# Kernel optimization log

Hardware: AMD Instinct MI355X
Metric: run time of the kernel (lower is better)

## Reference

```python
import jax, jax.numpy as jnp
import numpy as np

B, S, D, E, K = 4, 4096, 2048, 64, 2
LN_EPS = 1e-5
TEMP_EPS = 1e-6
Z_LOSS_COEF = 0.001
LB_COEF = 0.1


def setup_inputs() -> dict:
    key = jax.random.key(0)
    k1, k2 = jax.random.split(key)
    x = jax.random.normal(k1, (B, S, D), dtype=jnp.float32)
    # kaiming_normal fan_in (std = 1/sqrt(D)) scaled by 0.01, as in __init__
    W = jax.random.normal(k2, (E, D), dtype=jnp.float32) * jnp.float32(0.01 / np.sqrt(D))
    gamma = jnp.ones((E,), jnp.float32)   # LayerNorm weight
    beta = jnp.zeros((E,), jnp.float32)   # LayerNorm bias
    temperature = jnp.full((1,), 0.5, jnp.float32)
    return {"x": x, "W": W, "gamma": gamma, "beta": beta, "temperature": temperature}


def reference(x, W, gamma, beta, temperature):
    b, s, d = x.shape
    xf = x.reshape(-1, d)                                  # [N, D]
    logits = xf @ W.T                                      # [N, E]
    # LayerNorm over expert dim (biased variance, eps=1e-5, matches torch)
    mu = logits.mean(axis=-1, keepdims=True)
    var = jnp.mean(jnp.square(logits - mu), axis=-1, keepdims=True)
    logits = (logits - mu) * jax.lax.rsqrt(var + LN_EPS) * gamma + beta
    # temperature-scaled softmax
    routing_weights = jax.nn.softmax(logits / (temperature + TEMP_EPS), axis=-1)  # [N, E]
    # top-k + scatter into dense dispatch mask
    top_w, top_idx = jax.lax.top_k(routing_weights, K)     # [N, K]
    n = routing_weights.shape[0]
    dispatch = jnp.zeros_like(routing_weights).at[jnp.arange(n)[:, None], top_idx].set(top_w)
    dispatch = dispatch.reshape(b, s, E)                   # [B, S, E]
    # aux losses
    expert_load = dispatch.mean(axis=1)                    # [B, E]
    load_balance_loss = jnp.std(expert_load, ddof=1) / expert_load.mean() * 10.0
    router_z_loss = jnp.mean(jnp.square(logits))
    total_loss = ZLC * router_z_loss + LB_COEF * load_balance_loss if False else (
        Z_LOSS_COEF * router_z_loss + LB_COEF * load_balance_loss)
    return jax.lax.stop_gradient(routing_weights), dispatch, total_loss
```

## Files before the change

### kernel.cpp

```cpp
#include <hip/hip_runtime.h>
#include <hip/hip_bf16.h>
#include <float.h>
#include <math.h>

#define B_DIM 4
#define S_DIM 4096
#define D_DIM 2048
#define E_DIM 64
#define N_TOK 16384
#define TOKS 32
#define NBLK (N_TOK / TOKS)
#define NTHR 512
#define SLICES 4
#define DSLICE (D_DIM / SLICES)
#define KSTEPS2 16
#define GAP_THRESH 1e-3f
#define MAXFLAG 16

typedef __bf16 bf16x8_t __attribute__((ext_vector_type(8)));
typedef float f32x4_t __attribute__((ext_vector_type(4)));

union U8 { bf16x8_t v; unsigned short u[8]; };

__device__ __forceinline__ void split2(float f, unsigned short& h, unsigned short& l) {
    unsigned int u = __float_as_uint(f);
    h = (unsigned short)(u >> 16);
    float hf = __uint_as_float(u & 0xFFFF0000u);
    l = (unsigned short)(__float_as_uint(f - hf) >> 16);
}

typedef const __attribute__((address_space(1))) unsigned int* gas1_t;
typedef __attribute__((address_space(3))) unsigned int* las3_t;
__device__ __forceinline__ void gll16(const unsigned short* g, unsigned short* l) {
    __builtin_amdgcn_global_load_lds((gas1_t)(const void*)g, (las3_t)(void*)l, 16, 0, 0);
}

__global__ void wsplit(const float* __restrict__ W, unsigned short* __restrict__ wh,
                       unsigned short* __restrict__ wl, float* __restrict__ wshdr) {
    const int i = blockIdx.x * 256 + threadIdx.x;
    if (blockIdx.x == 0) { wshdr[threadIdx.x] = 0.f; wshdr[threadIdx.x + 256] = 0.f; }
    const int e    = i >> 8;
    const int k8   = i & 255;
    const int quad = k8 & 3;
    const int h    = (k8 >> 2) & 1;
    const int s    = (k8 >> 3) & 7;
    const int sl   = k8 >> 6;
    const int t    = e >> 4;
    const int l15  = e & 15;
    const int lane = quad * 16 + l15;
    const size_t f = ((size_t)((sl * 8 + s) * 2 + h) * 4 + t) * 64 + lane;
    float4 a = *(const float4*)(W + (size_t)e * D_DIM + k8 * 8);
    float4 b = *(const float4*)(W + (size_t)e * D_DIM + k8 * 8 + 4);
    ushort4 h0, l0, h1, l1;
    split2(a.x, h0.x, l0.x); split2(a.y, h0.y, l0.y);
    split2(a.z, h0.z, l0.z); split2(a.w, h0.w, l0.w);
    split2(b.x, h1.x, l1.x); split2(b.y, h1.y, l1.y);
    split2(b.z, h1.z, l1.z); split2(b.w, h1.w, l1.w);
    *(ushort4*)(wh + f * 8)     = h0;
    *(ushort4*)(wh + f * 8 + 4) = h1;
    *(ushort4*)(wl + f * 8)     = l0;
    *(ushort4*)(wl + f * 8 + 4) = l1;
}

__global__ __launch_bounds__(NTHR, 4) void router_main(
    const float* __restrict__ x, const float* __restrict__ W,
    const unsigned short* __restrict__ whg, const unsigned short* __restrict__ wlg,
    const float* __restrict__ gamma, const float* __restrict__ beta,
    const float* __restrict__ temperature,
    float* __restrict__ out_rw, float* __restrict__ out_dp,
    float* __restrict__ g_zsum, float* __restrict__ g_load)
{
    __shared__ __align__(16) unsigned char arena[65536];
    unsigned short* const bufH = (unsigned short*)arena;
    unsigned short* const bufL = (unsigned short*)(arena + 32768);
    float (* const part)[TOKS][E_DIM + 2] = (float (*)[TOKS][E_DIM + 2])arena;
    float (* const lgt)[E_DIM + 1] = (float (*)[E_DIM + 1])(arena + 33792);

    __shared__ float lgm[E_DIM], lbt[E_DIM], loadsum[E_DIM];
    __shared__ float smu[TOKS], srs[TOKS], sinv[TOKS];
    __shared__ int sel1[TOKS], sel2[TOKS];
    __shared__ int ftok[MAXFLAG], fcand[MAXFLAG][3];
    __shared__ int nflag;

    const int tid = threadIdx.x;
    const int tokBase = blockIdx.x * TOKS;
    const int lane = tid & 63;
    const int wv = tid >> 6;
    const int g  = wv & 1;
    const int sl = wv >> 1;
    const int l15 = lane & 15;
    const int quad = lane >> 4;

    if (tid == 0) nflag = 0;
    if (tid < E_DIM) { lgm[tid] = gamma[tid]; lbt[tid] = beta[tid]; loadsum[tid] = 0.f; }

    const float* xp = x + (size_t)(tokBase + g * 16 + l15) * D_DIM + sl * DSLICE + quad * 8;

    const int kk0  = tid >> 8;
    const int soff = (tid & 255) * 8;

    f32x4_t acc[4];
    #pragma unroll
    for (int t = 0; t < 4; ++t) acc[t] = (f32x4_t){0.f, 0.f, 0.f, 0.f};

#define STAGE(S2, B) do {                                                          \
        const size_t gof = (size_t)(S2) * 2048 + soff;                             \
        unsigned short* hB = bufH + (B) * 8192;                                    \
        unsigned short* lB = bufL + (B) * 8192;                                    \
        gll16(whg + (size_t)kk0 * 32768 + gof,       hB + kk0 * 2048 + soff);      \
        gll16(wlg + (size_t)kk0 * 32768 + gof,       lB + kk0 * 2048 + soff);      \
        gll16(whg + (size_t)(kk0 + 2) * 32768 + gof, hB + (kk0 + 2) * 2048 + soff);\
        gll16(wlg + (size_t)(kk0 + 2) * 32768 + gof, lB + (kk0 + 2) * 2048 + soff);\
    } while (0)

    STAGE(0, 0);
    float4 xq0 = *(const float4*)(xp);
    float4 xq1 = *(const float4*)(xp + 4);
    __syncthreads();

    for (int s2 = 0; s2 < KSTEPS2; ++s2) {
        const int cur = s2 & 1;
        const bool more = (s2 + 1 < KSTEPS2);
        float4 xn0, xn1;
        if (more) {
            STAGE(s2 + 1, cur ^ 1);
            xn0 = *(const float4*)(xp + (s2 + 1) * 32);
            xn1 = *(const float4*)(xp + (s2 + 1) * 32 + 4);
        }
        const unsigned short* hb = bufH + cur * 8192 + sl * 2048;
        const unsigned short* lb = bufL + cur * 8192 + sl * 2048;
        bf16x8_t bh[4], bl[4];
        #pragma unroll
        for (int t = 0; t < 4; ++t) {
            bh[t] = *(const bf16x8_t*)(hb + t * 512 + lane * 8);
            bl[t] = *(const bf16x8_t*)(lb + t * 512 + lane * 8);
        }
        float tf[8] = {xq0.x, xq0.y, xq0.z, xq0.w, xq1.x, xq1.y, xq1.z, xq1.w};
        U8 ah, al;
        #pragma unroll
        for (int k = 0; k < 8; ++k) split2(tf[k], ah.u[k], al.u[k]);
        #pragma unroll
        for (int t = 0; t < 4; ++t) {
            acc[t] = __builtin_amdgcn_mfma_f32_16x16x32_bf16(ah.v, bh[t], acc[t], 0, 0, 0);
            acc[t] = __builtin_amdgcn_mfma_f32_16x16x32_bf16(ah.v, bl[t], acc[t], 0, 0, 0);
            acc[t] = __builtin_amdgcn_mfma_f32_16x16x32_bf16(al.v, bh[t], acc[t], 0, 0, 0);
        }
        if (more) { xq0 = xn0; xq1 = xn1; }
        __syncthreads();
    }
#undef STAGE

    #pragma unroll
    for (int t = 0; t < 4; ++t)
        #pragma unroll
        for (int r = 0; r < 4; ++r)
            part[sl][g * 16 + quad * 4 + r][t * 16 + l15] = acc[t][r];
    __syncthreads();

    for (int i = tid; i < TOKS * E_DIM; i += NTHR) {
        int r = i >> 6, c = i & 63;
        lgt[r][c] = (part[0][r][c] + part[1][r][c]) + (part[2][r][c] + part[3][r][c]);
    }
    __syncthreads();

    if (wv < 2) {
        const int tok = wv * 16 + l15;
        const int q = quad;
        const float it = 1.f / (temperature[0] + 1e-6f);
        float s1 = 0.f, s2 = 0.f;
        #pragma unroll
        for (int e = 0; e < 16; ++e) { float v = lgt[tok][q * 16 + e]; s1 += v; s2 += v * v; }
        s1 += __shfl_xor(s1, 16); s1 += __shfl_xor(s1, 32);
        s2 += __shfl_xor(s2, 16); s2 += __shfl_xor(s2, 32);
        const float mu  = s1 * (1.f / 64.f);
        const float var = s2 * (1.f / 64.f) - mu * mu;
        const float rs  = rsqrtf(var + 1e-5f);
        if (q == 0) { smu[tok] = mu; srs[tok] = rs; }

        float m0 = -FLT_MAX, m1 = -FLT_MAX, m2 = -FLT_MAX;
        int   i0 = -1, i1 = -1, i2 = -1;
        float zl = 0.f;
        #pragma unroll
        for (int e = 0; e < 16; ++e) {
            int c = q * 16 + e;
            float y = (lgt[tok][c] - mu) * rs * lgm[c] + lbt[c];
            lgt[tok][c] = y;
            zl += y * y;
            if (y > m0)      { m2 = m1; i2 = i1; m1 = m0; i1 = i0; m0 = y; i0 = c; }
            else if (y > m1) { m2 = m1; i2 = i1; m1 = y; i1 = c; }
            else if (y > m2) { m2 = y; i2 = c; }
        }
        #pragma unroll
        for (int d = 16; d <= 32; d <<= 1) {
            float n0 = __shfl_xor(m0, d), n1 = __shfl_xor(m1, d), n2 = __shfl_xor(m2, d);
            int   j0 = __shfl_xor(i0, d), j1 = __shfl_xor(i1, d), j2 = __shfl_xor(i2, d);
            bool t0 = (m0 > n0) || (m0 == n0 && i0 < j0);
            float r0v = t0 ? m0 : n0; int r0i = t0 ? i0 : j0;
            float A0v = t0 ? m1 : m0; int A0i = t0 ? i1 : i0;
            float A1v = t0 ? m2 : m1; int A1i = t0 ? i2 : i1;
            float B0v = t0 ? n0 : n1; int B0i = t0 ? j0 : j1;
            float B1v = t0 ? n1 : n2; int B1i = t0 ? j1 : j2;
            bool t1 = (A0v > B0v) || (A0v == B0v && A0i < B0i);
            float r1v = t1 ? A0v : B0v; int r1i = t1 ? A0i : B0i;
            float A0w = t1 ? A1v : A0v; int A0j = t1 ? A1i : A0i;
            float B0w = t1 ? B0v : B1v; int B0j = t1 ? B0i : B1i;
            bool t2 = (A0w > B0w) || (A0w == B0w && A0j < B0j);
            float r2v = t2 ? A0w : B0w; int r2i = t2 ? A0j : B0j;
            m0 = r0v; i0 = r0i; m1 = r1v; i1 = r1i; m2 = r2v; i2 = r2i;
        }
        if (q == 0) {
            sel1[tok] = i0; sel2[tok] = i1;
            if (m1 - m2 < GAP_THRESH) {
                int sf = atomicAdd(&nflag, 1);
                if (sf < MAXFLAG) { ftok[sf] = tok; fcand[sf][0] = i0; fcand[sf][1] = i1; fcand[sf][2] = i2; }
            }
        }
        float es = 0.f;
        #pragma unroll
        for (int e = 0; e < 16; ++e) {
            int c = q * 16 + e;
            float ev = __expf((lgt[tok][c] - m0) * it);
            lgt[tok][c] = ev; es += ev;
        }
        es += __shfl_xor(es, 16); es += __shfl_xor(es, 32);
        if (q == 0) sinv[tok] = 1.f / es;
        zl += __shfl_xor(zl, 1); zl += __shfl_xor(zl, 2); zl += __shfl_xor(zl, 4);
        zl += __shfl_xor(zl, 8); zl += __shfl_xor(zl, 16); zl += __shfl_xor(zl, 32);
        if (lane == 0) atomicAdd(g_zsum, zl);
    }
    __syncthreads();

    const int nf = min(nflag, MAXFLAG);
    for (int f = wv; f < nf; f += 8) {
        const int tk = ftok[f];
        const int c0 = fcand[f][0], c1 = fcand[f][1], c2 = fcand[f][2];
        const float* xr = x + (size_t)(tokBase + tk) * D_DIM;
        const float* w0 = W + (size_t)c0 * D_DIM;
        const float* w1 = W + (size_t)c1 * D_DIM;
        const float* w2 = W + (size_t)c2 * D_DIM;
        double L0 = 0.0, L1 = 0.0, L2 = 0.0;
        for (int i = lane; i < D_DIM; i += 64) {
            double xv = (double)xr[i];
            L0 += xv * (double)w0[i];
            L1 += xv * (double)w1[i];
            L2 += xv * (double)w2[i];
        }
        #pragma unroll
        for (int off = 32; off; off >>= 1) {
            L0 += __shfl_down(L0, off);
            L1 += __shfl_down(L1, off);
            L2 += __shfl_down(L2, off);
        }
        if (lane == 0) {
            double dmu = (double)smu[tk], drs = (double)srs[tk];
            double y0 = (L0 - dmu) * drs * (double)lgm[c0] + (double)lbt[c0];
            double y1 = (L1 - dmu) * drs * (double)lgm[c1] + (double)lbt[c1];
            double y2 = (L2 - dmu) * drs * (double)lgm[c2] + (double)lbt[c2];
            bool g01 = (y0 > y1) || (y0 == y1 && c0 < c1);
            bool g02 = (y0 > y2) || (y0 == y2 && c0 < c2);
            bool g12 = (y1 > y2) || (y1 == y2 && c1 < c2);
            int a, b;
            if (!g01 && !g02)      { a = c1; b = c2; }
            else if (g01 && !g12)  { a = c0; b = c2; }
            else                   { a = c0; b = c1; }
            sel1[tk] = a; sel2[tk] = b;
        }
    }
    __syncthreads();

    if (tid < TOKS) {
        float inv = sinv[tid];
        atomicAdd(&loadsum[sel1[tid]], lgt[tid][sel1[tid]] * inv);
        atomicAdd(&loadsum[sel2[tid]], lgt[tid][sel2[tid]] * inv);
    }
    __syncthreads();
    if (tid < E_DIM) atomicAdd(&g_load[(tokBase >> 12) * E_DIM + tid], loadsum[tid]);

    float* orw = out_rw + (size_t)tokBase * E_DIM;
    float* odp = out_dp + (size_t)tokBase * E_DIM;
    for (int i = tid; i < TOKS * E_DIM; i += NTHR) {
        int r = i >> 6, c = i & 63;
        float p = lgt[r][c] * sinv[r];
        orw[i] = p;
        odp[i] = (c == sel1[r] || c == sel2[r]) ? p : 0.f;
    }
}

__global__ void router_fin(const float* __restrict__ ws, float* __restrict__ out_loss) {
    __shared__ float sv[B_DIM * E_DIM];
    const int tid = threadIdx.x;
    sv[tid] = ws[8 + tid] * (1.f / S_DIM);
    __syncthreads();
    if (tid == 0) {
        float s = 0.f;
        for (int i = 0; i < B_DIM * E_DIM; ++i) s += sv[i];
        const float mean = s * (1.f / (B_DIM * E_DIM));
        float ss = 0.f;
        for (int i = 0; i < B_DIM * E_DIM; ++i) { float d = sv[i] - mean; ss += d * d; }
        const float sd = sqrtf(ss * (1.f / (B_DIM * E_DIM - 1)));
        const float z = ws[0] * (1.f / ((float)N_TOK * E_DIM));
        out_loss[0] = 0.001f * z + 0.1f * (sd / mean) * 10.f;
    }
}

extern "C" void kernel_launch(void* const* d_in, const int* in_sizes, int n_in,
                              void* d_out, int out_size, void* d_ws, size_t ws_size,
                              hipStream_t stream) {
    const float* x     = (const float*)d_in[0];
    const float* W     = (const float*)d_in[1];
    const float* gamma = (const float*)d_in[2];
    const float* beta  = (const float*)d_in[3];
    const float* temp  = (const float*)d_in[4];
    float* out  = (float*)d_out;
    float* rw   = out;
    float* dp   = out + (size_t)N_TOK * E_DIM;
    float* loss = out + 2 * (size_t)N_TOK * E_DIM;
    float* ws   = (float*)d_ws;

    unsigned short* whg = (unsigned short*)((char*)d_ws + 4096);
    unsigned short* wlg = whg + (size_t)E_DIM * D_DIM;

    wsplit<<<dim3(64), dim3(256), 0, stream>>>(W, whg, wlg, ws);
    router_main<<<dim3(NBLK), dim3(NTHR), 0, stream>>>(x, W, whg, wlg, gamma, beta, temp,
                                                       rw, dp, ws, ws + 8);
    router_fin<<<dim3(1), dim3(256), 0, stream>>>(ws, loss);
}
```

Measured before the change: 233.1 us.

## Prefetch W tiles two stages ahead with explicit vmcnt waits and raw barriers

```diff
diff --git a/kernel.cpp b/kernel.cpp
--- a/kernel.cpp
+++ b/kernel.cpp
@@ -114,18 +114,21 @@
     } while (0)
 
     STAGE(0, 0);
-    float4 xq0 = *(const float4*)(xp);
-    float4 xq1 = *(const float4*)(xp + 4);
-    __syncthreads();
-
+    float4 xqA0 = *(const float4*)(xp);
+    float4 xqA1 = *(const float4*)(xp + 4);
+    STAGE(1, 1);
+    asm volatile("s_waitcnt vmcnt(6)" ::: "memory");
+    __builtin_amdgcn_sched_barrier(0);
+    __builtin_amdgcn_s_barrier();
+
+    float4 xqB0, xqB1;
+    #pragma unroll
     for (int s2 = 0; s2 < KSTEPS2; ++s2) {
         const int cur = s2 & 1;
-        const bool more = (s2 + 1 < KSTEPS2);
-        float4 xn0, xn1;
-        if (more) {
-            STAGE(s2 + 1, cur ^ 1);
-            xn0 = *(const float4*)(xp + (s2 + 1) * 32);
-            xn1 = *(const float4*)(xp + (s2 + 1) * 32 + 4);
+        if (s2 + 1 < KSTEPS2) {
+            const float* xg = xp + (s2 + 1) * 32;
+            xqB0 = *(const float4*)(xg);
+            xqB1 = *(const float4*)(xg + 4);
         }
         const unsigned short* hb = bufH + cur * 8192 + sl * 2048;
         const unsigned short* lb = bufL + cur * 8192 + sl * 2048;
@@ -135,7 +138,7 @@
             bh[t] = *(const bf16x8_t*)(hb + t * 512 + lane * 8);
             bl[t] = *(const bf16x8_t*)(lb + t * 512 + lane * 8);
         }
-        float tf[8] = {xq0.x, xq0.y, xq0.z, xq0.w, xq1.x, xq1.y, xq1.z, xq1.w};
+        float tf[8] = {xqA0.x, xqA0.y, xqA0.z, xqA0.w, xqA1.x, xqA1.y, xqA1.z, xqA1.w};
         U8 ah, al;
         #pragma unroll
         for (int k = 0; k < 8; ++k) split2(tf[k], ah.u[k], al.u[k]);
@@ -145,10 +148,20 @@
             acc[t] = __builtin_amdgcn_mfma_f32_16x16x32_bf16(ah.v, bl[t], acc[t], 0, 0, 0);
             acc[t] = __builtin_amdgcn_mfma_f32_16x16x32_bf16(al.v, bh[t], acc[t], 0, 0, 0);
         }
-        if (more) { xq0 = xn0; xq1 = xn1; }
-        __syncthreads();
+        __builtin_amdgcn_s_barrier();
+        if (s2 + 2 < KSTEPS2) {
+            STAGE(s2 + 2, cur);
+            asm volatile("s_waitcnt vmcnt(6)" ::: "memory");
+        } else if (s2 + 1 < KSTEPS2) {
+            asm volatile("s_waitcnt vmcnt(2)" ::: "memory");
+        }
+        __builtin_amdgcn_sched_barrier(0);
+        __builtin_amdgcn_s_barrier();
+        xqA0 = xqB0; xqA1 = xqB1;
     }
 #undef STAGE
+
+    __syncthreads();
 
     #pragma unroll
     for (int t = 0; t < 4; ++t)
```

New measurement: 227.1 us (median of 2 runs). -2.6%, faster.

## Halve block to four waves, each covering both token groups with private W staging

Applied to the files above, without the earlier changes.

```diff
diff --git a/kernel.cpp b/kernel.cpp
--- a/kernel.cpp
+++ b/kernel.cpp
@@ -10,7 +10,7 @@
 #define N_TOK 16384
 #define TOKS 32
 #define NBLK (N_TOK / TOKS)
-#define NTHR 512
+#define NTHR 256
 #define SLICES 4
 #define DSLICE (D_DIM / SLICES)
 #define KSTEPS2 16
@@ -62,7 +62,7 @@
     *(ushort4*)(wl + f * 8 + 4) = l1;
 }
 
-__global__ __launch_bounds__(NTHR, 4) void router_main(
+__global__ __launch_bounds__(NTHR, 2) void router_main(
     const float* __restrict__ x, const float* __restrict__ W,
     const unsigned short* __restrict__ whg, const unsigned short* __restrict__ wlg,
     const float* __restrict__ gamma, const float* __restrict__ beta,
@@ -86,75 +86,94 @@
     const int tokBase = blockIdx.x * TOKS;
     const int lane = tid & 63;
     const int wv = tid >> 6;
-    const int g  = wv & 1;
-    const int sl = wv >> 1;
     const int l15 = lane & 15;
     const int quad = lane >> 4;
 
     if (tid == 0) nflag = 0;
     if (tid < E_DIM) { lgm[tid] = gamma[tid]; lbt[tid] = beta[tid]; loadsum[tid] = 0.f; }
 
-    const float* xp = x + (size_t)(tokBase + g * 16 + l15) * D_DIM + sl * DSLICE + quad * 8;
-
-    const int kk0  = tid >> 8;
-    const int soff = (tid & 255) * 8;
-
-    f32x4_t acc[4];
+    const float* xp0 = x + (size_t)(tokBase + l15) * D_DIM      + wv * DSLICE + quad * 8;
+    const float* xp1 = x + (size_t)(tokBase + 16 + l15) * D_DIM + wv * DSLICE + quad * 8;
+
+    const unsigned short* hsrc0 = whg + (size_t)wv * 16 * 2048 + lane * 8;
+    const unsigned short* lsrc0 = wlg + (size_t)wv * 16 * 2048 + lane * 8;
+    unsigned short* const hdst0 = bufH + wv * 2 * 2048 + lane * 8;
+    unsigned short* const ldst0 = bufL + wv * 2 * 2048 + lane * 8;
+
+#define STAGE(S2, B) do {                                                   \
+        const unsigned short* hs = hsrc0 + (size_t)(S2) * 2048;             \
+        const unsigned short* ls = lsrc0 + (size_t)(S2) * 2048;             \
+        unsigned short* hd = hdst0 + (B) * 2048;                            \
+        unsigned short* ld = ldst0 + (B) * 2048;                            \
+        gll16(hs,        hd);        gll16(ls,        ld);                  \
+        gll16(hs +  512, hd +  512); gll16(ls +  512, ld +  512);           \
+        gll16(hs + 1024, hd + 1024); gll16(ls + 1024, ld + 1024);           \
+        gll16(hs + 1536, hd + 1536); gll16(ls + 1536, ld + 1536);           \
+    } while (0)
+
+    f32x4_t acc[2][4];
     #pragma unroll
-    for (int t = 0; t < 4; ++t) acc[t] = (f32x4_t){0.f, 0.f, 0.f, 0.f};
-
-#define STAGE(S2, B) do {                                                          \
-        const size_t gof = (size_t)(S2) * 2048 + soff;                             \
-        unsigned short* hB = bufH + (B) * 8192;                                    \
-        unsigned short* lB = bufL + (B) * 8192;                                    \
-        gll16(whg + (size_t)kk0 * 32768 + gof,       hB + kk0 * 2048 + soff);      \
-        gll16(wlg + (size_t)kk0 * 32768 + gof,       lB + kk0 * 2048 + soff);      \
-        gll16(whg + (size_t)(kk0 + 2) * 32768 + gof, hB + (kk0 + 2) * 2048 + soff);\
-        gll16(wlg + (size_t)(kk0 + 2) * 32768 + gof, lB + (kk0 + 2) * 2048 + soff);\
-    } while (0)
+    for (int m = 0; m < 2; ++m)
+        #pragma unroll
+        for (int t = 0; t < 4; ++t) acc[m][t] = (f32x4_t){0.f, 0.f, 0.f, 0.f};
 
     STAGE(0, 0);
-    float4 xq0 = *(const float4*)(xp);
-    float4 xq1 = *(const float4*)(xp + 4);
-    __syncthreads();
+    float4 xqA[4], xqB[4];
+    xqA[0] = *(const float4*)(xp0);  xqA[1] = *(const float4*)(xp0 + 4);
+    xqA[2] = *(const float4*)(xp1);  xqA[3] = *(const float4*)(xp1 + 4);
+    asm volatile("s_waitcnt vmcnt(0)" ::: "memory");
+    __builtin_amdgcn_sched_barrier(0);
 
     for (int s2 = 0; s2 < KSTEPS2; ++s2) {
         const int cur = s2 & 1;
         const bool more = (s2 + 1 < KSTEPS2);
-        float4 xn0, xn1;
         if (more) {
             STAGE(s2 + 1, cur ^ 1);
-            xn0 = *(const float4*)(xp + (s2 + 1) * 32);
-            xn1 = *(const float4*)(xp + (s2 + 1) * 32 + 4);
-        }
-        const unsigned short* hb = bufH + cur * 8192 + sl * 2048;
-        const unsigned short* lb = bufL + cur * 8192 + sl * 2048;
+            const float* xg0 = xp0 + (s2 + 1) * 32;
+            const float* xg1 = xp1 + (s2 + 1) * 32;
+            xqB[0] = *(const float4*)(xg0);  xqB[1] = *(const float4*)(xg0 + 4);
+            xqB[2] = *(const float4*)(xg1);  xqB[3] = *(const float4*)(xg1 + 4);
+        }
+        const unsigned short* hb = bufH + (wv * 2 + cur) * 2048;
+        const unsigned short* lb = bufL + (wv * 2 + cur) * 2048;
         bf16x8_t bh[4], bl[4];
         #pragma unroll
         for (int t = 0; t < 4; ++t) {
             bh[t] = *(const bf16x8_t*)(hb + t * 512 + lane * 8);
             bl[t] = *(const bf16x8_t*)(lb + t * 512 + lane * 8);
         }
-        float tf[8] = {xq0.x, xq0.y, xq0.z, xq0.w, xq1.x, xq1.y, xq1.z, xq1.w};
-        U8 ah, al;
-        #pragma unroll
-        for (int k = 0; k < 8; ++k) split2(tf[k], ah.u[k], al.u[k]);
-        #pragma unroll
-        for (int t = 0; t < 4; ++t) {
-            acc[t] = __builtin_amdgcn_mfma_f32_16x16x32_bf16(ah.v, bh[t], acc[t], 0, 0, 0);
-            acc[t] = __builtin_amdgcn_mfma_f32_16x16x32_bf16(ah.v, bl[t], acc[t], 0, 0, 0);
-            acc[t] = __builtin_amdgcn_mfma_f32_16x16x32_bf16(al.v, bh[t], acc[t], 0, 0, 0);
-        }
-        if (more) { xq0 = xn0; xq1 = xn1; }
-        __syncthreads();
+        #pragma unroll
+        for (int m = 0; m < 2; ++m) {
+            float tf[8] = {xqA[m*2].x, xqA[m*2].y, xqA[m*2].z, xqA[m*2].w,
+                           xqA[m*2+1].x, xqA[m*2+1].y, xqA[m*2+1].z, xqA[m*2+1].w};
+            U8 ah, al;
+            #pragma unroll
+            for (int k = 0; k < 8; ++k) split2(tf[k], ah.u[k], al.u[k]);
+            #pragma unroll
+            for (int t = 0; t < 4; ++t) {
+                acc[m][t] = __builtin_amdgcn_mfma_f32_16x16x32_bf16(ah.v, bh[t], acc[m][t], 0, 0, 0);
+                acc[m][t] = __builtin_amdgcn_mfma_f32_16x16x32_bf16(ah.v, bl[t], acc[m][t], 0, 0, 0);
+                acc[m][t] = __builtin_amdgcn_mfma_f32_16x16x32_bf16(al.v, bh[t], acc[m][t], 0, 0, 0);
+            }
+        }
+        if (more) {
+            asm volatile("s_waitcnt vmcnt(0)" ::: "memory");
+            __builtin_amdgcn_sched_barrier(0);
+            #pragma unroll
+            for (int j = 0; j < 4; ++j) xqA[j] = xqB[j];
+        }
     }
 #undef STAGE
 
+    __syncthreads();
+
     #pragma unroll
-    for (int t = 0; t < 4; ++t)
-        #pragma unroll
-        for (int r = 0; r < 4; ++r)
-            part[sl][g * 16 + quad * 4 + r][t * 16 + l15] = acc[t][r];
+    for (int m = 0; m < 2; ++m)
+        #pragma unroll
+        for (int t = 0; t < 4; ++t)
+            #pragma unroll
+            for (int r = 0; r < 4; ++r)
+                part[wv][m * 16 + quad * 4 + r][t * 16 + l15] = acc[m][t][r];
     __syncthreads();
 
     for (int i = tid; i < TOKS * E_DIM; i += NTHR) {
@@ -231,7 +250,7 @@
     __syncthreads();
 
     const int nf = min(nflag, MAXFLAG);
-    for (int f = wv; f < nf; f += 8) {
+    for (int f = wv; f < nf; f += 4) {
         const int tk = ftok[f];
         const int c0 = fcand[f][0], c1 = fcand[f][1], c2 = fcand[f][2];
         const float* xr = x + (size_t)(tokBase + tk) * D_DIM;
```

Result: no change. 234.7 us (+0.6%).
